# Performance work log

Measured on AMD Instinct MI355X. Metric: run time of the kernel, lower is better.

The kernel has to match this reference:

```python
import jax, jax.numpy as jnp
import numpy as np

B, N, M, D = 256, 256, 256, 1024
BIG = 1e30  # stands in for +inf; far larger than any reachable DTW cost (<= 2*N)


def setup_inputs() -> dict:
    key = jax.random.key(0)
    k1, k2 = jax.random.split(key)
    seq1 = jax.random.normal(k1, (B, N, D), dtype=jnp.float32)
    seq2 = jax.random.normal(k2, (B, M, D), dtype=jnp.float32)
    return {"seq1": seq1, "seq2": seq2}


def _cosine_distance(x, y):
    # F.normalize(p=2, dim=2) with eps=1e-12, then 1 - clamp(x_n @ y_n^T, -1, 1)
    xn = x / jnp.maximum(jnp.linalg.norm(x, axis=2, keepdims=True), 1e-12)
    yn = y / jnp.maximum(jnp.linalg.norm(y, axis=2, keepdims=True), 1e-12)
    sim = jnp.einsum('bnd,bmd->bnm', xn, yn)
    return 1.0 - jnp.clip(sim, -1.0, 1.0)


def _dtw(dist, band_radius):
    # Banded (Sakoe-Chiba) DTW DP: acc[i,j] = d[i,j] + min(acc[i-1,j], acc[i,j-1], acc[i-1,j-1])
    # Row-wise lax.scan; within-row recurrence a[j] = min(b[j], a[j-1] + s[j]) is a
    # min-plus linear recurrence, solved in parallel with lax.associative_scan.
    b, n, m = dist.shape
    jdx = jnp.arange(m)
    # row 0: cumulative sum inside band (j <= r), BIG outside
    row0 = jnp.where(jdx[None, :] <= band_radius, jnp.cumsum(dist[:, 0, :], axis=1), BIG)

    def step(prev, xs):
        i, di = xs  # di: [b, m] = dist[:, i, :]
        in_band = (jdx >= 1) & (jdx >= i - band_radius) & (jdx <= i + band_radius)
        # column 0 only initialized while i <= band_radius (matches torch loop)
        a0 = jnp.where(i <= band_radius, prev[:, 0] + di[:, 0], BIG)
        prev_shift = jnp.concatenate([jnp.full((b, 1), BIG, dist.dtype), prev[:, :-1]], axis=1)
        c = jnp.minimum(prev, prev_shift)  # min(acc[i-1,j], acc[i-1,j-1])
        bt = jnp.where(in_band[None, :], c + di, BIG)
        st = jnp.where(in_band[None, :], di, BIG)

        def comb(l, r):
            sl, tl = l
            sr, tr = r
            return (sl + sr, jnp.minimum(tr, tl + sr))

        ss, tt = jax.lax.associative_scan(comb, (st[:, 1:], bt[:, 1:]), axis=1)
        row = jnp.concatenate([a0[:, None], jnp.minimum(tt, a0[:, None] + ss)], axis=1)
        return row, None

    xs = (jnp.arange(1, n), jnp.swapaxes(dist[:, 1:, :], 0, 1))  # ([n-1], [n-1,b,m])
    last_row, _ = jax.lax.scan(step, row0, xs)
    return last_row[:, m - 1]


def reference(seq1, seq2):
    dist = _cosine_distance(seq1, seq2)
    band_radius = min(N, M) // 2  # default: half of shorter sequence
    return _dtw(dist, band_radius)
```

## Files before the change

### kernel.cpp

```cpp
#include <hip/hip_runtime.h>
#include <hip/hip_bf16.h>

#define B_ 256
#define N_ 256
#define M_ 256
#define D_ 1024
#define RAD 128
#define BIGF 1e30f

typedef short bf16x8 __attribute__((ext_vector_type(8)));
typedef float f32x4 __attribute__((ext_vector_type(4)));

__device__ __forceinline__ short f2bf(float f) {
    __hip_bfloat16 h = __float2bfloat16(f);
    return __builtin_bit_cast(short, h);
}

__device__ __forceinline__ void cvt4(const float4 v, short* s, float& n) {
    n += v.x * v.x + v.y * v.y + v.z * v.z + v.w * v.w;
    s[0] = f2bf(v.x); s[1] = f2bf(v.y); s[2] = f2bf(v.z); s[3] = f2bf(v.w);
}

__global__ __launch_bounds__(256) void gemm_dist_kernel(
        const float* __restrict__ X, const float* __restrict__ Y,
        float* __restrict__ dist) {
    const int bid = blockIdx.x;
    const int b  = bid >> 2;
    const int ti = (bid >> 1) & 1;
    const int tj = bid & 1;

    __shared__ short As[128][32];
    __shared__ short Bs[128][32];
    __shared__ float redA[256];
    __shared__ float redB[256];
    __shared__ float rnx[128];
    __shared__ float rny[128];

    const int t    = threadIdx.x;
    const int row  = t >> 1;
    const int kh   = (t & 1) << 4;
    const int wave = t >> 6;
    const int lane = t & 63;
    const int wi   = (wave >> 1) << 6;
    const int wj   = (wave & 1) << 6;
    const int fq   = lane >> 4;
    const int fr   = lane & 15;

    const float* ax = X + (((size_t)b * N_ + ti * 128 + row) * D_) + kh;
    const float* by = Y + (((size_t)b * M_ + tj * 128 + row) * D_) + kh;

    f32x4 acc[4][4];
    const f32x4 zero = {0.f, 0.f, 0.f, 0.f};
#pragma unroll
    for (int r = 0; r < 4; ++r)
#pragma unroll
        for (int c = 0; c < 4; ++c) acc[r][c] = zero;

    float nA = 0.f, nB = 0.f;

    for (int kt = 0; kt < D_ / 32; ++kt) {
        const float4 va0 = *(const float4*)(ax + 0);
        const float4 va1 = *(const float4*)(ax + 4);
        const float4 va2 = *(const float4*)(ax + 8);
        const float4 va3 = *(const float4*)(ax + 12);
        const float4 vb0 = *(const float4*)(by + 0);
        const float4 vb1 = *(const float4*)(by + 4);
        const float4 vb2 = *(const float4*)(by + 8);
        const float4 vb3 = *(const float4*)(by + 12);
        ax += 32; by += 32;

        short sa[16], sb[16];
        cvt4(va0, sa + 0,  nA); cvt4(va1, sa + 4,  nA);
        cvt4(va2, sa + 8,  nA); cvt4(va3, sa + 12, nA);
        cvt4(vb0, sb + 0,  nB); cvt4(vb1, sb + 4,  nB);
        cvt4(vb2, sb + 8,  nB); cvt4(vb3, sb + 12, nB);

        __syncthreads();
        *(bf16x8*)&As[row][kh]     = *(bf16x8*)&sa[0];
        *(bf16x8*)&As[row][kh + 8] = *(bf16x8*)&sa[8];
        *(bf16x8*)&Bs[row][kh]     = *(bf16x8*)&sb[0];
        *(bf16x8*)&Bs[row][kh + 8] = *(bf16x8*)&sb[8];
        __syncthreads();

        bf16x8 af[4], bf[4];
#pragma unroll
        for (int r = 0; r < 4; ++r)
            af[r] = *(const bf16x8*)&As[wi + r * 16 + fr][fq * 8];
#pragma unroll
        for (int c = 0; c < 4; ++c)
            bf[c] = *(const bf16x8*)&Bs[wj + c * 16 + fr][fq * 8];
#pragma unroll
        for (int r = 0; r < 4; ++r)
#pragma unroll
            for (int c = 0; c < 4; ++c)
                acc[r][c] = __builtin_amdgcn_mfma_f32_16x16x32_bf16(
                    af[r], bf[c], acc[r][c], 0, 0, 0);
    }

    redA[t] = nA;
    redB[t] = nB;
    __syncthreads();
    if (t < 128) {
        float sA = redA[2 * t] + redA[2 * t + 1];
        float sB = redB[2 * t] + redB[2 * t + 1];
        rnx[t] = 1.0f / fmaxf(sqrtf(sA), 1e-12f);
        rny[t] = 1.0f / fmaxf(sqrtf(sB), 1e-12f);
    }
    __syncthreads();

    float* Dp = dist + (((size_t)b * N_ + ti * 128) * M_) + tj * 128;
#pragma unroll
    for (int r = 0; r < 4; ++r) {
#pragma unroll
        for (int c = 0; c < 4; ++c) {
            const int col = wj + c * 16 + fr;
            const float rc = rny[col];
#pragma unroll
            for (int g = 0; g < 4; ++g) {
                const int rw = wi + r * 16 + fq * 4 + g;
                float v = acc[r][c][g] * rnx[rw] * rc;
                v = fminf(1.0f, fmaxf(-1.0f, v));
                Dp[(size_t)rw * M_ + col] = 1.0f - v;
            }
        }
    }
}

__global__ __launch_bounds__(64) void dtw_kernel(
        const float* __restrict__ dist, float* __restrict__ out) {
    const int b = blockIdx.x;
    const int lane = threadIdx.x;
    const float* Db = dist + (size_t)b * N_ * M_;
    const int j0 = lane << 2;

    float4 d = *(const float4*)(Db + j0);
    float s0 = d.x, s1 = s0 + d.y, s2 = s1 + d.z, s3 = s2 + d.w;
    float tot = s3;
#pragma unroll
    for (int off = 1; off < 64; off <<= 1) {
        float o = __shfl_up(tot, off);
        if (lane >= off) tot += o;
    }
    float excl = __shfl_up(tot, 1);
    if (lane == 0) excl = 0.f;
    float prev[4];
    prev[0] = (j0 + 0 <= RAD) ? excl + s0 : BIGF;
    prev[1] = (j0 + 1 <= RAD) ? excl + s1 : BIGF;
    prev[2] = (j0 + 2 <= RAD) ? excl + s2 : BIGF;
    prev[3] = (j0 + 3 <= RAD) ? excl + s3 : BIGF;

    float4 dn = *(const float4*)(Db + M_ + j0);

    for (int i = 1; i < N_; ++i) {
        d = dn;
        if (i + 1 < N_) dn = *(const float4*)(Db + (size_t)(i + 1) * M_ + j0);

        const float pm1 = __shfl_up(prev[3], 1);
        const float p00 = __shfl(prev[0], 0);
        const float d00 = __shfl(d.x, 0);
        const float a0 = (i <= RAD) ? p00 + d00 : BIGF;

        const float de[4] = {d.x, d.y, d.z, d.w};
        const float ps[4] = {pm1, prev[0], prev[1], prev[2]};

        float S = 0.f, T = BIGF;
        float Se[4], Te[4];
#pragma unroll
        for (int e = 0; e < 4; ++e) {
            const int j = j0 + e;
            float st, bt;
            if (j == 0) {
                st = 0.f; bt = BIGF;
            } else {
                const bool in = (j >= i - RAD) && (j <= i + RAD);
                const float c = fminf(prev[e], ps[e]);
                bt = in ? c + de[e] : BIGF;
                st = in ? de[e] : BIGF;
            }
            T = fminf(bt, T + st);
            S = S + st;
            Se[e] = S; Te[e] = T;
        }

        float iS = S, iT = T;
#pragma unroll
        for (int off = 1; off < 64; off <<= 1) {
            float oS = __shfl_up(iS, off);
            float oT = __shfl_up(iT, off);
            if (lane >= off) {
                iT = fminf(iT, oT + iS);
                iS = oS + iS;
            }
        }
        float eS = __shfl_up(iS, 1);
        float eT = __shfl_up(iT, 1);
        if (lane == 0) { eS = 0.f; eT = BIGF; }

#pragma unroll
        for (int e = 0; e < 4; ++e) {
            const float fS = eS + Se[e];
            const float fT = fminf(Te[e], eT + Se[e]);
            prev[e] = fminf(fT, a0 + fS);
        }
        if (lane == 0) prev[0] = a0;
    }

    if (lane == 63) out[b] = prev[3];
}

extern "C" void kernel_launch(void* const* d_in, const int* in_sizes, int n_in,
                              void* d_out, int out_size, void* d_ws, size_t ws_size,
                              hipStream_t stream) {
    const float* seq1 = (const float*)d_in[0];
    const float* seq2 = (const float*)d_in[1];
    float* out = (float*)d_out;
    float* dist = (float*)d_ws;

    hipLaunchKernelGGL(gemm_dist_kernel, dim3(B_ * 4), dim3(256), 0, stream,
                       seq1, seq2, dist);
    hipLaunchKernelGGL(dtw_kernel, dim3(B_), dim3(64), 0, stream, dist, out);
}
```

Before: 655.5 us.

## Prefetch next K-tile into registers, pad LDS, skip out-of-band waves in GEMM

The cosine-distance GEMM now loads the next K-slice of X and Y into registers before the MFMA work on the current slice, so global-load latency overlaps compute. Shared tiles are padded to 40 shorts per row to reduce LDS bank conflicts, and the kernel gets an occupancy hint. Waves whose 64x64 sub-tile lies entirely outside the Sakoe-Chiba band skip their MFMAs and stores. Stores are also masked to in-band cells only, and the norm reduction uses a lane shuffle instead of shared-memory arrays. The costs are more register pressure and unwritten workspace entries outside the band, which the DTW kernel masks anyway.

After: 680.8 us. 3.9% more time.

```diff
diff --git a/kernel.cpp b/kernel.cpp
--- a/kernel.cpp
+++ b/kernel.cpp
@@ -7,6 +7,7 @@
 #define D_ 1024
 #define RAD 128
 #define BIGF 1e30f
+#define LDK 40
 
 typedef short bf16x8 __attribute__((ext_vector_type(8)));
 typedef float f32x4 __attribute__((ext_vector_type(4)));
@@ -21,7 +22,7 @@
     s[0] = f2bf(v.x); s[1] = f2bf(v.y); s[2] = f2bf(v.z); s[3] = f2bf(v.w);
 }
 
-__global__ __launch_bounds__(256) void gemm_dist_kernel(
+__global__ __launch_bounds__(256, 3) void gemm_dist_kernel(
         const float* __restrict__ X, const float* __restrict__ Y,
         float* __restrict__ dist) {
     const int bid = blockIdx.x;
@@ -29,10 +30,8 @@
     const int ti = (bid >> 1) & 1;
     const int tj = bid & 1;
 
-    __shared__ short As[128][32];
-    __shared__ short Bs[128][32];
-    __shared__ float redA[256];
-    __shared__ float redB[256];
+    __shared__ short As[128][LDK];
+    __shared__ short Bs[128][LDK];
     __shared__ float rnx[128];
     __shared__ float rny[128];
 
@@ -46,6 +45,9 @@
     const int fq   = lane >> 4;
     const int fr   = lane & 15;
 
+    const int gi0 = ti * 128 + wi, gj0 = tj * 128 + wj;
+    const bool deadwave = (gj0 > gi0 + 63 + RAD) || (gj0 + 63 < gi0 - RAD);
+
     const float* ax = X + (((size_t)b * N_ + ti * 128 + row) * D_) + kh;
     const float* by = Y + (((size_t)b * M_ + tj * 128 + row) * D_) + kh;
 
@@ -58,23 +60,23 @@
 
     float nA = 0.f, nB = 0.f;
 
+    float4 va0 = *(const float4*)(ax + 0);
+    float4 va1 = *(const float4*)(ax + 4);
+    float4 va2 = *(const float4*)(ax + 8);
+    float4 va3 = *(const float4*)(ax + 12);
+    float4 vb0 = *(const float4*)(by + 0);
+    float4 vb1 = *(const float4*)(by + 4);
+    float4 vb2 = *(const float4*)(by + 8);
+    float4 vb3 = *(const float4*)(by + 12);
+    ax += 32; by += 32;
+
+    short sa[16], sb[16];
+    cvt4(va0, sa + 0,  nA); cvt4(va1, sa + 4,  nA);
+    cvt4(va2, sa + 8,  nA); cvt4(va3, sa + 12, nA);
+    cvt4(vb0, sb + 0,  nB); cvt4(vb1, sb + 4,  nB);
+    cvt4(vb2, sb + 8,  nB); cvt4(vb3, sb + 12, nB);
+
     for (int kt = 0; kt < D_ / 32; ++kt) {
-        const float4 va0 = *(const float4*)(ax + 0);
-        const float4 va1 = *(const float4*)(ax + 4);
-        const float4 va2 = *(const float4*)(ax + 8);
-        const float4 va3 = *(const float4*)(ax + 12);
-        const float4 vb0 = *(const float4*)(by + 0);
-        const float4 vb1 = *(const float4*)(by + 4);
-        const float4 vb2 = *(const float4*)(by + 8);
-        const float4 vb3 = *(const float4*)(by + 12);
-        ax += 32; by += 32;
-
-        short sa[16], sb[16];
-        cvt4(va0, sa + 0,  nA); cvt4(va1, sa + 4,  nA);
-        cvt4(va2, sa + 8,  nA); cvt4(va3, sa + 12, nA);
-        cvt4(vb0, sb + 0,  nB); cvt4(vb1, sb + 4,  nB);
-        cvt4(vb2, sb + 8,  nB); cvt4(vb3, sb + 12, nB);
-
         __syncthreads();
         *(bf16x8*)&As[row][kh]     = *(bf16x8*)&sa[0];
         *(bf16x8*)&As[row][kh + 8] = *(bf16x8*)&sa[8];
@@ -82,45 +84,72 @@
         *(bf16x8*)&Bs[row][kh + 8] = *(bf16x8*)&sb[8];
         __syncthreads();
 
-        bf16x8 af[4], bf[4];
-#pragma unroll
-        for (int r = 0; r < 4; ++r)
-            af[r] = *(const bf16x8*)&As[wi + r * 16 + fr][fq * 8];
-#pragma unroll
-        for (int c = 0; c < 4; ++c)
-            bf[c] = *(const bf16x8*)&Bs[wj + c * 16 + fr][fq * 8];
-#pragma unroll
-        for (int r = 0; r < 4; ++r)
+        const bool more = (kt < D_ / 32 - 1);
+        if (more) {
+            va0 = *(const float4*)(ax + 0);
+            va1 = *(const float4*)(ax + 4);
+            va2 = *(const float4*)(ax + 8);
+            va3 = *(const float4*)(ax + 12);
+            vb0 = *(const float4*)(by + 0);
+            vb1 = *(const float4*)(by + 4);
+            vb2 = *(const float4*)(by + 8);
+            vb3 = *(const float4*)(by + 12);
+            ax += 32; by += 32;
+        }
+
+        if (!deadwave) {
+            bf16x8 af[4], bg[4];
+#pragma unroll
+            for (int r = 0; r < 4; ++r)
+                af[r] = *(const bf16x8*)&As[wi + r * 16 + fr][fq * 8];
 #pragma unroll
             for (int c = 0; c < 4; ++c)
-                acc[r][c] = __builtin_amdgcn_mfma_f32_16x16x32_bf16(
-                    af[r], bf[c], acc[r][c], 0, 0, 0);
-    }
-
-    redA[t] = nA;
-    redB[t] = nB;
+                bg[c] = *(const bf16x8*)&Bs[wj + c * 16 + fr][fq * 8];
+#pragma unroll
+            for (int r = 0; r < 4; ++r)
+#pragma unroll
+                for (int c = 0; c < 4; ++c)
+                    acc[r][c] = __builtin_amdgcn_mfma_f32_16x16x32_bf16(
+                        af[r], bg[c], acc[r][c], 0, 0, 0);
+        }
+
+        if (more) {
+            cvt4(va0, sa + 0,  nA); cvt4(va1, sa + 4,  nA);
+            cvt4(va2, sa + 8,  nA); cvt4(va3, sa + 12, nA);
+            cvt4(vb0, sb + 0,  nB); cvt4(vb1, sb + 4,  nB);
+            cvt4(vb2, sb + 8,  nB); cvt4(vb3, sb + 12, nB);
+        }
+    }
+
+    const float nAs = nA + __shfl_xor(nA, 1);
+    const float nBs = nB + __shfl_xor(nB, 1);
+    if ((t & 1) == 0) {
+        rnx[row] = 1.0f / fmaxf(sqrtf(nAs), 1e-12f);
+        rny[row] = 1.0f / fmaxf(sqrtf(nBs), 1e-12f);
+    }
     __syncthreads();
-    if (t < 128) {
-        float sA = redA[2 * t] + redA[2 * t + 1];
-        float sB = redB[2 * t] + redB[2 * t + 1];
-        rnx[t] = 1.0f / fmaxf(sqrtf(sA), 1e-12f);
-        rny[t] = 1.0f / fmaxf(sqrtf(sB), 1e-12f);
-    }
-    __syncthreads();
-
-    float* Dp = dist + (((size_t)b * N_ + ti * 128) * M_) + tj * 128;
-#pragma unroll
-    for (int r = 0; r < 4; ++r) {
-#pragma unroll
-        for (int c = 0; c < 4; ++c) {
-            const int col = wj + c * 16 + fr;
-            const float rc = rny[col];
-#pragma unroll
-            for (int g = 0; g < 4; ++g) {
-                const int rw = wi + r * 16 + fq * 4 + g;
-                float v = acc[r][c][g] * rnx[rw] * rc;
-                v = fminf(1.0f, fmaxf(-1.0f, v));
-                Dp[(size_t)rw * M_ + col] = 1.0f - v;
+
+    if (!deadwave) {
+        float* Dp = dist + (((size_t)b * N_ + ti * 128) * M_) + tj * 128;
+#pragma unroll
+        for (int r = 0; r < 4; ++r) {
+#pragma unroll
+            for (int c = 0; c < 4; ++c) {
+                const int col = wj + c * 16 + fr;
+                const int gj  = tj * 128 + col;
+                const float rc = rny[col];
+#pragma unroll
+                for (int g = 0; g < 4; ++g) {
+                    const int rw = wi + r * 16 + fq * 4 + g;
+                    const int gi = ti * 128 + rw;
+                    const bool keep = (gi == 0) ? (gj <= RAD)
+                                    : (gj <= gi + RAD && gj >= gi - RAD);
+                    if (keep) {
+                        float v = acc[r][c][g] * rnx[rw] * rc;
+                        v = fminf(1.0f, fmaxf(-1.0f, v));
+                        Dp[(size_t)rw * M_ + col] = 1.0f - v;
+                    }
+                }
             }
         }
     }
```
